# Kernel tuning notes

Hardware: AMD Instinct MI355X
Metric: run time of the kernel (lower is better)

The kernel has to match this reference:

```python
import jax, jax.numpy as jnp
import numpy as np
from jax import lax

B, H, W = 128, 128, 128
CHANS = [3, 32, 64, 128]   # convolution_structure
F, FH, FW = 128, 16, 16    # n_features, feature map size after 3 maxpools
P = FH * FW                # flatten_feature_size = 256
E, OUT = 32, 53            # expert_output_len, output_len


def _conv(x, w, b):
    # NCHW conv, 3x3, SAME padding, stride 1
    y = lax.conv_general_dilated(x, w, (1, 1), 'SAME',
                                 dimension_numbers=('NCHW', 'OIHW', 'NCHW'))
    return y + b[None, :, None, None]


def _maxpool2(x):
    return lax.reduce_window(x, -jnp.inf, lax.max,
                             (1, 1, 2, 2), (1, 1, 2, 2), 'VALID')


def setup_inputs() -> dict:
    key = jax.random.key(0)
    ks = jax.random.split(key, 16)

    def n(k, shape, fan_in):
        return jax.random.normal(k, shape, jnp.float32) / np.float32(np.sqrt(fan_in))

    inp = {'x': jax.random.normal(ks[0], (B, CHANS[0], H, W), jnp.float32)}
    for i in range(3):
        cin, cout = CHANS[i], CHANS[i + 1]
        inp[f'cw{i + 1}'] = n(ks[1 + i], (cout, cin, 3, 3), cin * 9)
        inp[f'cb{i + 1}'] = jnp.zeros((cout,), jnp.float32)
    inp['Wa'] = n(ks[4], (F, P), P)
    inp['ba'] = jnp.zeros((F,), jnp.float32)
    # per-expert MLP 256 -> 256 -> 128 -> 32 (128 experts, batched)
    inp['ew1'] = n(ks[5], (F, 256, 256), 256)
    inp['eb1'] = jnp.zeros((F, 256), jnp.float32)
    inp['ew2'] = n(ks[6], (F, 256, 128), 256)
    inp['eb2'] = jnp.zeros((F, 128), jnp.float32)
    inp['ew3'] = n(ks[7], (F, 128, E), 128)
    inp['eb3'] = jnp.zeros((F, E), jnp.float32)
    inp['fw'] = n(ks[8], (F * E, OUT), F * E)
    inp['fb'] = jnp.zeros((OUT,), jnp.float32)
    return inp


def reference(x, cw1, cb1, cw2, cb2, cw3, cb3, Wa, ba,
              ew1, eb1, ew2, eb2, ew3, eb3, fw, fb):
    # CNNBlock: (conv3x3 + ReLU + maxpool2) x 3  -> [B, F, 16, 16]
    h = x
    for w, b in ((cw1, cb1), (cw2, cb2), (cw3, cb3)):
        h = _maxpool2(jax.nn.relu(_conv(h, w, b)))
    feat = h.reshape(h.shape[0], F, P)                        # [B, F, 256]

    # AttentionBlock: per-feature scalar gate (attention_value = 1)
    att = jax.nn.sigmoid(jnp.einsum('bfp,fp->bf', feat, Wa) + ba)[:, :, None]

    # Experts: 128 independent gated MLPs, batched as grouped GEMMs
    z = feat * att                                            # input gating
    z = jax.nn.relu(jnp.einsum('bfp,fpq->bfq', z, ew1) + eb1)
    z = jax.nn.relu(jnp.einsum('bfp,fpq->bfq', z, ew2) + eb2)
    z = jnp.einsum('bfp,fpq->bfq', z, ew3) + eb3              # [B, F, 32]

    # outer ReLU over stacked expert outputs, flatten, final dense (att=1)
    z = jax.nn.relu(z).reshape(z.shape[0], -1)                # [B, 4096]
    return z @ fw + fb                                        # [B, 53]
```

## Files before the change

kernel.cpp:

```cpp
#include <hip/hip_runtime.h>
#include <hip/hip_bf16.h>
#include <math.h>

#define NF 128
#define NP 256

typedef __attribute__((ext_vector_type(8))) short bf16x8;
typedef __attribute__((ext_vector_type(4))) short bf16x4;
typedef __attribute__((ext_vector_type(4))) float f32x4;

#define GLOBAL_AS __attribute__((address_space(1)))
#define LDS_AS __attribute__((address_space(3)))

__global__ void __launch_bounds__(256) packs_k(
    const float* __restrict__ cw1, const float* __restrict__ cw2,
    const float* __restrict__ cw3, const float* __restrict__ fw,
    __hip_bfloat16* __restrict__ wp1, __hip_bfloat16* __restrict__ wp2,
    __hip_bfloat16* __restrict__ wp3, float* __restrict__ fwt)
{
    const int bid = blockIdx.x, tid = threadIdx.x;
    if (bid < 8) {
        int i = bid * 256 + tid;
        if (i >= 2048) return;
        int s = i >> 10, co = (i >> 5) & 31, k = i & 31;
        int o = s * 8 + (k >> 2), ch = k & 3;
        float v = 0.f;
        if (o < 9 && ch < 3) v = cw1[(size_t)(co * 3 + ch) * 9 + o];
        wp1[i] = __float2bfloat16(v);
    } else if (bid < 80) {
        int i = (bid - 8) * 256 + tid;
        if (i >= 9 * 64 * 32) return;
        int o = i / 2048, r = i - o * 2048;
        int co = r >> 5, ci = r & 31;
        wp2[i] = __float2bfloat16(cw2[(size_t)(co * 32 + ci) * 9 + o]);
    } else if (bid < 368) {
        int i = (bid - 80) * 256 + tid;
        if (i >= 9 * 128 * 64) return;
        int o = i / 8192, r = i - o * 8192;
        int co = r >> 6, ci = r & 63;
        wp3[i] = __float2bfloat16(cw3[(size_t)(co * 64 + ci) * 9 + o]);
    } else {
        int i = (bid - 368) * 256 + tid;
        if (i >= 53 * 4096) return;
        int o = i >> 12, k = i & 4095;
        fwt[i] = fw[(size_t)k * 53 + o];
    }
}

__global__ void __launch_bounds__(256) tpack_k(const float* __restrict__ in,
                                               __hip_bfloat16* __restrict__ out,
                                               int P, int Q, int qtiles)
{
    const int f  = blockIdx.y;
    const int pt = blockIdx.x / qtiles, qt = blockIdx.x - pt * qtiles;
    __shared__ float t[32][33];
    const float* src = in + (size_t)f * P * Q;
    __hip_bfloat16* dst = out + (size_t)f * P * Q;
    const int rr = threadIdx.x >> 5, c = threadIdx.x & 31;
    #pragma unroll
    for (int i = 0; i < 4; ++i)
        t[rr + i * 8][c] = src[(size_t)(pt * 32 + rr + i * 8) * Q + qt * 32 + c];
    __syncthreads();
    #pragma unroll
    for (int i = 0; i < 4; ++i)
        dst[(size_t)(qt * 32 + rr + i * 8) * P + pt * 32 + c] =
            __float2bfloat16(t[c][rr + i * 8]);
}

__global__ void __launch_bounds__(256, 2) conv1_mfma(
    const float* __restrict__ x,
    const __hip_bfloat16* __restrict__ wp1,
    const float* __restrict__ bias,
    __hip_bfloat16* __restrict__ out)
{
    __shared__ char lds[14 * 130 * 8];
    const int rb  = blockIdx.x * 8;
    const int b   = blockIdx.z;
    const int tid = threadIdx.x;

    #pragma unroll
    for (int t = 0; t < 8; ++t) {
        int u = tid + t * 256;
        if (u < 14 * 130) {
            int px = u % 130, row = u / 130;
            int gy = rb + row - 1, gx = px - 1;
            unsigned short hv[4] = {0, 0, 0, 0};
            if (gy >= 0 && gy < 128 && gx >= 0 && gx < 128) {
                size_t base = (((size_t)b * 3) * 128 + gy) * 128 + gx;
                __hip_bfloat16 h0 = __float2bfloat16(x[base]);
                __hip_bfloat16 h1 = __float2bfloat16(x[base + 16384]);
                __hip_bfloat16 h2 = __float2bfloat16(x[base + 32768]);
                __builtin_memcpy(&hv[0], &h0, 2);
                __builtin_memcpy(&hv[1], &h1, 2);
                __builtin_memcpy(&hv[2], &h2, 2);
            }
            *(int2*)(lds + u * 8) = *(const int2*)hv;
        }
    }
    __syncthreads();

    const int w = tid >> 6, lane = tid & 63, p = lane & 15, q = lane >> 4;

    f32x4 acc[16][2];
    #pragma unroll
    for (int m = 0; m < 16; ++m)
        #pragma unroll
        for (int n = 0; n < 2; ++n) {
            acc[m][n][0] = 0.f; acc[m][n][1] = 0.f;
            acc[m][n][2] = 0.f; acc[m][n][3] = 0.f;
        }

    #pragma unroll
    for (int s = 0; s < 2; ++s) {
        bf16x8 bfr[2];
        #pragma unroll
        for (int n = 0; n < 2; ++n)
            bfr[n] = *(const bf16x8*)(wp1 + (size_t)(s * 32 + n * 16 + p) * 32 + q * 8);
        const int o0 = s * 8 + q * 2, o1 = o0 + 1;
        const int dy0 = o0 / 3, dx0 = o0 - 3 * dy0;
        const int dy1 = o1 / 3, dx1 = o1 - 3 * dy1;
        #pragma unroll
        for (int m = 0; m < 16; ++m) {
            const int mr = m >> 3, mx = m & 7;
            const int r0 = (2 * w + mr + dy0) * 130 + mx * 16 + p + dx0;
            const int r1 = (2 * w + mr + dy1) * 130 + mx * 16 + p + dx1;
            bf16x4 lo = *(const bf16x4*)(lds + r0 * 8);
            bf16x4 hi = *(const bf16x4*)(lds + r1 * 8);
            bf16x8 afr = __builtin_shufflevector(lo, hi, 0, 1, 2, 3, 4, 5, 6, 7);
            #pragma unroll
            for (int n = 0; n < 2; ++n)
                acc[m][n] = __builtin_amdgcn_mfma_f32_16x16x32_bf16(afr, bfr[n], acc[m][n], 0, 0, 0);
        }
    }

    const int prow = (rb >> 1) + w;
    float bv[2] = { bias[p], bias[16 + p] };
    #pragma unroll
    for (int mx = 0; mx < 8; ++mx)
        #pragma unroll
        for (int n = 0; n < 2; ++n) {
            f32x4 lo = acc[mx][n], hi = acc[8 + mx][n];
            float v0 = fmaxf(fmaxf(fmaxf(lo[0], lo[1]), fmaxf(hi[0], hi[1])) + bv[n], 0.f);
            float v1 = fmaxf(fmaxf(fmaxf(lo[2], lo[3]), fmaxf(hi[2], hi[3])) + bv[n], 0.f);
            int px = mx * 8 + q * 2;
            size_t base = ((size_t)(b * 64 + prow) * 64 + px) * 32 + n * 16 + p;
            out[base]      = __float2bfloat16(v0);
            out[base + 32] = __float2bfloat16(v1);
        }
}

template<int W, int CIN, int COUT, int SWZ, int OUTF>
__global__ void __launch_bounds__(256, 2) conv_mfma(
    const __hip_bfloat16* __restrict__ in,
    const __hip_bfloat16* __restrict__ wp,
    const float* __restrict__ bias,
    __hip_bfloat16* __restrict__ outb,
    float* __restrict__ outf)
{
    constexpr int XW  = W / 16;
    constexpr int AF  = 2 * XW;
    constexpr int BF  = COUT / 16;
    constexpr int CH  = CIN / 8;
    constexpr int KH  = CIN / 32;
    constexpr int NSTEP = 9 * KH;
    constexpr int PXW = W + 2;
    constexpr int UNITS  = 10 * PXW * CH;
    constexpr int NIT    = (UNITS + 255) / 256;
    constexpr int STAGEB = UNITS * 16;
    constexpr int OUTLDS = OUTF ? (COUT * 68 * 4) : 0;
    constexpr int LDSB   = STAGEB > OUTLDS ? STAGEB : OUTLDS;

    __shared__ int4 ldsv[(LDSB + 15) / 16];
    char* ldsc = (char*)ldsv;

    const int rb  = blockIdx.x * 8;
    const int b   = blockIdx.z;
    const int tid = threadIdx.x;
    const int w = tid >> 6, lane = tid & 63, p = lane & 15, q = lane >> 4;

    #pragma unroll
    for (int t = 0; t < NIT; ++t) {
        int u = tid + t * 256;
        if (u < UNITS) {
            int ch = u % CH; int pl = u / CH;
            int xx = pl % PXW; int row = pl / PXW;
            int gy = rb + row - 1, gx = xx - 1;
            if (gy >= 0 && gy < W && gx >= 0 && gx < W) {
                int ch_src = SWZ ? (ch ^ (pl & 7)) : ch;
                const __hip_bfloat16* gp = in + ((size_t)(b * W + gy) * W + gx) * CIN + ch_src * 8;
                char* lb = ldsc + (size_t)(t * 256 + (tid & ~63)) * 16;
                __builtin_amdgcn_global_load_lds(
                    (const GLOBAL_AS void*)gp, (LDS_AS void*)lb, 16, 0, 0);
            } else {
                *(int4*)(ldsc + (size_t)u * 16) = make_int4(0, 0, 0, 0);
            }
        }
    }

    bf16x8 bcur[BF], bnxt[BF];
    #pragma unroll
    for (int n = 0; n < BF; ++n)
        bcur[n] = *(const bf16x8*)(wp + (size_t)(n * 16 + p) * CIN + q * 8);

    __syncthreads();

    f32x4 acc[AF][BF];
    #pragma unroll
    for (int m = 0; m < AF; ++m)
        #pragma unroll
        for (int n = 0; n < BF; ++n) {
            acc[m][n][0] = 0.f; acc[m][n][1] = 0.f;
            acc[m][n][2] = 0.f; acc[m][n][3] = 0.f;
        }

    float bv[BF];
    #pragma unroll
    for (int n = 0; n < BF; ++n) bv[n] = bias[n * 16 + p];

    #pragma unroll 1
    for (int s = 0; s < NSTEP; ++s) {
        const int o  = (KH == 1) ? s : (s >> 1);
        const int h  = (KH == 1) ? 0 : (s & 1);
        const int ky = o / 3, kx = o - 3 * (o / 3);

        if (s + 1 < NSTEP) {
            const int o2 = (KH == 1) ? (s + 1) : ((s + 1) >> 1);
            const int h2 = (KH == 1) ? 0 : ((s + 1) & 1);
            #pragma unroll
            for (int n = 0; n < BF; ++n)
                bnxt[n] = *(const bf16x8*)(wp + (size_t)(o2 * COUT + n * 16 + p) * CIN + h2 * 32 + q * 8);
        }

        bf16x8 afr[AF];
        #pragma unroll
        for (int m = 0; m < AF; ++m) {
            const int mr = m / XW, mx = m % XW;
            const int pix = (2 * w + mr + ky) * PXW + mx * 16 + kx + p;
            const int ch = h * 4 + q;
            const int slot = SWZ ? (pix * CH + (ch ^ (pix & 7))) : (pix * CH + ch);
            afr[m] = *(const bf16x8*)(ldsc + slot * 16);
        }
        #pragma unroll
        for (int m = 0; m < AF; ++m)
            #pragma unroll
            for (int n = 0; n < BF; ++n)
                acc[m][n] = __builtin_amdgcn_mfma_f32_16x16x32_bf16(afr[m], bcur[n], acc[m][n], 0, 0, 0);

        #pragma unroll
        for (int n = 0; n < BF; ++n) bcur[n] = bnxt[n];
    }

    const int prow = (rb >> 1) + w;
    if constexpr (OUTF == 0) {
        #pragma unroll
        for (int mx = 0; mx < XW; ++mx)
            #pragma unroll
            for (int n = 0; n < BF; ++n) {
                f32x4 lo = acc[mx][n], hi = acc[XW + mx][n];
                float v0 = fmaxf(fmaxf(fmaxf(lo[0], lo[1]), fmaxf(hi[0], hi[1])) + bv[n], 0.f);
                float v1 = fmaxf(fmaxf(fmaxf(lo[2], lo[3]), fmaxf(hi[2], hi[3])) + bv[n], 0.f);
                int px = mx * 8 + q * 2;
                size_t base = ((size_t)(b * (W / 2) + prow) * (W / 2) + px) * COUT + n * 16 + p;
                outb[base]        = __float2bfloat16(v0);
                outb[base + COUT] = __float2bfloat16(v1);
            }
    } else {
        __syncthreads();
        float* fl = (float*)ldsc;
        #pragma unroll
        for (int mx = 0; mx < XW; ++mx)
            #pragma unroll
            for (int n = 0; n < BF; ++n) {
                f32x4 lo = acc[mx][n], hi = acc[XW + mx][n];
                float v0 = fmaxf(fmaxf(fmaxf(lo[0], lo[1]), fmaxf(hi[0], hi[1])) + bv[n], 0.f);
                float v1 = fmaxf(fmaxf(fmaxf(lo[2], lo[3]), fmaxf(hi[2], hi[3])) + bv[n], 0.f);
                int px = mx * 8 + q * 2;
                fl[(n * 16 + p) * 68 + w * 16 + px]     = v0;
                fl[(n * 16 + p) * 68 + w * 16 + px + 1] = v1;
            }
        __syncthreads();
        for (int i = tid; i < COUT * 16; i += 256) {
            int c = i >> 4, j4 = i & 15;
            float4 vv = *(const float4*)&fl[c * 68 + j4 * 4];
            *(float4*)(outf + (size_t)(b * COUT + c) * 256 + (rb >> 1) * 16 + j4 * 4) = vv;
        }
    }
}

__global__ void __launch_bounds__(256, 2) experts_mfma(
    const float* __restrict__ feat, const float* __restrict__ Wa,
    const float* __restrict__ ba,
    const __hip_bfloat16* __restrict__ w1, const float* __restrict__ eb1,
    const __hip_bfloat16* __restrict__ w2, const float* __restrict__ eb2,
    const __hip_bfloat16* __restrict__ w3, const float* __restrict__ eb3,
    float* __restrict__ z)
{
    const int f  = blockIdx.x;
    const int r0 = blockIdx.y * 32;
    const int tid = threadIdx.x;

    __shared__ __attribute__((aligned(16))) char lds[33024];
    char* Xb  = lds;
    char* H1b = lds + 16384;
    char* H2b = lds;
    float* attL = (float*)(lds + 32768);

    for (int u = tid; u < 32 * 32; u += 256) {
        int row = u >> 5, ch = u & 31;
        int b = r0 + row;
        const float* src = feat + ((size_t)b * NF + f) * NP + ch * 8;
        float4 v0 = *(const float4*)src;
        float4 v1 = *(const float4*)(src + 4);
        unsigned short hv[8];
        float vv[8] = {v0.x, v0.y, v0.z, v0.w, v1.x, v1.y, v1.z, v1.w};
        #pragma unroll
        for (int j = 0; j < 8; ++j) {
            __hip_bfloat16 hb = __float2bfloat16(vv[j]);
            __builtin_memcpy(&hv[j], &hb, 2);
        }
        int slot = row * 32 + (ch ^ (row & 7));
        *(int4*)(Xb + slot * 16) = *(const int4*)hv;
    }

    {
        int row = tid >> 3, g = tid & 7;
        const float* fr = feat + ((size_t)(r0 + row) * NF + f) * NP + g * 32;
        const float* wr = Wa + (size_t)f * NP + g * 32;
        float s = 0.f;
        #pragma unroll
        for (int j = 0; j < 32; j += 4) {
            float4 a  = *(const float4*)(fr + j);
            float4 w4 = *(const float4*)(wr + j);
            s += a.x * w4.x + a.y * w4.y + a.z * w4.z + a.w * w4.w;
        }
        s += __shfl_xor(s, 1);
        s += __shfl_xor(s, 2);
        s += __shfl_xor(s, 4);
        if (g == 0) attL[row] = 1.f / (1.f + expf(-(s + ba[f])));
    }
    __syncthreads();

    const int wv = tid >> 6, lane = tid & 63, p = lane & 15, q = lane >> 4;
    const int rh = wv & 1, cf = wv >> 1;
    const int mrow = rh * 16;

    f32x4 acc1[8];
    #pragma unroll
    for (int n = 0; n < 8; ++n) { acc1[n][0]=0.f; acc1[n][1]=0.f; acc1[n][2]=0.f; acc1[n][3]=0.f; }
    #pragma unroll
    for (int k = 0; k < 8; ++k) {
        bf16x8 bfr[8];
        #pragma unroll
        for (int n = 0; n < 8; ++n)
            bfr[n] = *(const bf16x8*)(w1 + ((size_t)f * 256 + cf * 128 + n * 16 + p) * 256 + k * 32 + q * 8);
        int row = mrow + p, ch = k * 4 + q;
        bf16x8 afr = *(const bf16x8*)(Xb + (row * 32 + (ch ^ (row & 7))) * 16);
        #pragma unroll
        for (int n = 0; n < 8; ++n)
            acc1[n] = __builtin_amdgcn_mfma_f32_16x16x32_bf16(afr, bfr[n], acc1[n], 0, 0, 0);
    }
    #pragma unroll
    for (int n = 0; n < 8; ++n) {
        int col = cf * 128 + n * 16 + p;
        float bb = eb1[(size_t)f * 256 + col];
        #pragma unroll
        for (int reg = 0; reg < 4; ++reg) {
            int row = mrow + q * 4 + reg;
            float v = fmaxf(attL[row] * acc1[n][reg] + bb, 0.f);
            int slot = row * 32 + ((col >> 3) ^ (row & 7));
            *(__hip_bfloat16*)(H1b + slot * 16 + (col & 7) * 2) = __float2bfloat16(v);
        }
    }
    __syncthreads();

    f32x4 acc2[4];
    #pragma unroll
    for (int n = 0; n < 4; ++n) { acc2[n][0]=0.f; acc2[n][1]=0.f; acc2[n][2]=0.f; acc2[n][3]=0.f; }
    #pragma unroll
    for (int k = 0; k < 8; ++k) {
        bf16x8 bfr[4];
        #pragma unroll
        for (int n = 0; n < 4; ++n)
            bfr[n] = *(const bf16x8*)(w2 + ((size_t)f * 128 + cf * 64 + n * 16 + p) * 256 + k * 32 + q * 8);
        int row = mrow + p, ch = k * 4 + q;
        bf16x8 afr = *(const bf16x8*)(H1b + (row * 32 + (ch ^ (row & 7))) * 16);
        #pragma unroll
        for (int n = 0; n < 4; ++n)
            acc2[n] = __builtin_amdgcn_mfma_f32_16x16x32_bf16(afr, bfr[n], acc2[n], 0, 0, 0);
    }
    #pragma unroll
    for (int n = 0; n < 4; ++n) {
        int col = cf * 64 + n * 16 + p;
        float bb = eb2[(size_t)f * 128 + col];
        #pragma unroll
        for (int reg = 0; reg < 4; ++reg) {
            float v = fmaxf(acc2[n][reg] + bb, 0.f);
            int row = mrow + q * 4 + reg;
            int slot = row * 16 + ((col >> 3) ^ (row & 7));
            *(__hip_bfloat16*)(H2b + slot * 16 + (col & 7) * 2) = __float2bfloat16(v);
        }
    }
    __syncthreads();

    f32x4 acc3;
    acc3[0]=0.f; acc3[1]=0.f; acc3[2]=0.f; acc3[3]=0.f;
    #pragma unroll
    for (int k = 0; k < 4; ++k) {
        bf16x8 bfr = *(const bf16x8*)(w3 + ((size_t)f * 32 + cf * 16 + p) * 128 + k * 32 + q * 8);
        int row = mrow + p, ch = k * 4 + q;
        bf16x8 afr = *(const bf16x8*)(H2b + (row * 16 + (ch ^ (row & 7))) * 16);
        acc3 = __builtin_amdgcn_mfma_f32_16x16x32_bf16(afr, bfr, acc3, 0, 0, 0);
    }
    {
        float bb = eb3[(size_t)f * 32 + cf * 16 + p];
        #pragma unroll
        for (int reg = 0; reg < 4; ++reg) {
            float v = fmaxf(acc3[reg] + bb, 0.f);
            int row = r0 + mrow + q * 4 + reg;
            z[(size_t)row * 4096 + f * 32 + cf * 16 + p] = v;
        }
    }
}

__global__ void __launch_bounds__(256) final_k(
    const float* __restrict__ z, const float* __restrict__ fwt,
    const float* __restrict__ fb, float* __restrict__ out)
{
    const int b  = blockIdx.x;
    const int og = blockIdx.y;
    __shared__ float zs[4096];
    for (int i = threadIdx.x; i < 1024; i += 256)
        *(float4*)&zs[i * 4] = *(const float4*)&z[(size_t)b * 4096 + i * 4];
    __syncthreads();

    const int wv = threadIdx.x >> 6, lane = threadIdx.x & 63;
    const int o = og * 4 + wv;
    if (o >= 53) return;
    const float4* wr = (const float4*)&fwt[(size_t)o * 4096];
    float s = 0.f;
    #pragma unroll
    for (int it = 0; it < 16; ++it) {
        float4 zv = *(const float4*)&zs[(it * 64 + lane) * 4];
        float4 w4 = wr[it * 64 + lane];
        s += zv.x * w4.x + zv.y * w4.y + zv.z * w4.z + zv.w * w4.w;
    }
    #pragma unroll
    for (int off = 32; off; off >>= 1) s += __shfl_down(s, off);
    if (lane == 0) out[b * 53 + o] = s + fb[o];
}

extern "C" void kernel_launch(void* const* d_in, const int* in_sizes, int n_in,
                              void* d_out, int out_size, void* d_ws, size_t ws_size,
                              hipStream_t stream)
{
    const float* x   = (const float*)d_in[0];
    const float* cw1 = (const float*)d_in[1];
    const float* cb1 = (const float*)d_in[2];
    const float* cw2 = (const float*)d_in[3];
    const float* cb2 = (const float*)d_in[4];
    const float* cw3 = (const float*)d_in[5];
    const float* cb3 = (const float*)d_in[6];
    const float* Wa  = (const float*)d_in[7];
    const float* ba  = (const float*)d_in[8];
    const float* ew1 = (const float*)d_in[9];
    const float* eb1 = (const float*)d_in[10];
    const float* ew2 = (const float*)d_in[11];
    const float* eb2 = (const float*)d_in[12];
    const float* ew3 = (const float*)d_in[13];
    const float* eb3 = (const float*)d_in[14];
    const float* fw  = (const float*)d_in[15];
    const float* fb  = (const float*)d_in[16];

    float* ws = (float*)d_ws;
    __hip_bfloat16* p1b  = (__hip_bfloat16*)ws;
    __hip_bfloat16* p2b  = (__hip_bfloat16*)(ws + 8388608);
    float* feat = ws + 12582912;
    __hip_bfloat16* wp2  = (__hip_bfloat16*)(ws + 16793600);
    __hip_bfloat16* wp3  = (__hip_bfloat16*)(ws + 16802816);
    __hip_bfloat16* ew1b = (__hip_bfloat16*)(ws + 16839680);
    __hip_bfloat16* ew2b = (__hip_bfloat16*)(ws + 21033984);
    __hip_bfloat16* ew3b = (__hip_bfloat16*)(ws + 23131136);
    float* fwt = ws + 23393280;
    __hip_bfloat16* wp1b = (__hip_bfloat16*)(ws + 23610368);
    float* z   = ws;

    packs_k<<<1216, 256, 0, stream>>>(cw1, cw2, cw3, fw, wp1b, wp2, wp3, fwt);
    tpack_k<<<dim3(64, 128), 256, 0, stream>>>(ew1, ew1b, 256, 256, 8);
    tpack_k<<<dim3(32, 128), 256, 0, stream>>>(ew2, ew2b, 256, 128, 4);
    tpack_k<<<dim3(4, 128), 256, 0, stream>>>(ew3, ew3b, 128, 32, 1);

    conv1_mfma<<<dim3(16, 1, 128), 256, 0, stream>>>(x, wp1b, cb1, p1b);
    conv_mfma<64, 32, 64, 0, 0><<<dim3(8, 1, 128), 256, 0, stream>>>(p1b, wp2, cb2, p2b, nullptr);
    conv_mfma<32, 64, 128, 1, 1><<<dim3(4, 1, 128), 256, 0, stream>>>(p2b, wp3, cb3, nullptr, feat);
    experts_mfma<<<dim3(128, 4), 256, 0, stream>>>(feat, Wa, ba, ew1b, eb1, ew2b, eb2, ew3b, eb3, z);
    final_k<<<dim3(128, 14), 256, 0, stream>>>(z, fwt, fb, (float*)d_out);
}
```

Measured before the change: 152.3 us.

## Merge weight-packing launches and widen expert tiles to 64 rows per block

```diff
diff --git a/kernel.cpp b/kernel.cpp
--- a/kernel.cpp
+++ b/kernel.cpp
@@ -12,12 +12,33 @@
 #define GLOBAL_AS __attribute__((address_space(1)))
 #define LDS_AS __attribute__((address_space(3)))
 
+__device__ __forceinline__ void tpack_tile(const float* __restrict__ src,
+                                           __hip_bfloat16* __restrict__ dst,
+                                           int P, int Q, int pt, int qt,
+                                           int tid, float (*t)[33])
+{
+    const int rr = tid >> 5, c = tid & 31;
+    #pragma unroll
+    for (int i = 0; i < 4; ++i)
+        t[rr + i * 8][c] = src[(size_t)(pt * 32 + rr + i * 8) * Q + qt * 32 + c];
+    __syncthreads();
+    #pragma unroll
+    for (int i = 0; i < 4; ++i)
+        dst[(size_t)(qt * 32 + rr + i * 8) * P + pt * 32 + c] =
+            __float2bfloat16(t[c][rr + i * 8]);
+}
+
 __global__ void __launch_bounds__(256) packs_k(
     const float* __restrict__ cw1, const float* __restrict__ cw2,
     const float* __restrict__ cw3, const float* __restrict__ fw,
+    const float* __restrict__ ew1, const float* __restrict__ ew2,
+    const float* __restrict__ ew3,
     __hip_bfloat16* __restrict__ wp1, __hip_bfloat16* __restrict__ wp2,
-    __hip_bfloat16* __restrict__ wp3, float* __restrict__ fwt)
-{
+    __hip_bfloat16* __restrict__ wp3, float* __restrict__ fwt,
+    __hip_bfloat16* __restrict__ ew1b, __hip_bfloat16* __restrict__ ew2b,
+    __hip_bfloat16* __restrict__ ew3b)
+{
+    __shared__ float t[32][33];
     const int bid = blockIdx.x, tid = threadIdx.x;
     if (bid < 8) {
         int i = bid * 256 + tid;
@@ -39,32 +60,27 @@
         int o = i / 8192, r = i - o * 8192;
         int co = r >> 6, ci = r & 63;
         wp3[i] = __float2bfloat16(cw3[(size_t)(co * 64 + ci) * 9 + o]);
-    } else {
+    } else if (bid < 1216) {
         int i = (bid - 368) * 256 + tid;
         if (i >= 53 * 4096) return;
         int o = i >> 12, k = i & 4095;
         fwt[i] = fw[(size_t)k * 53 + o];
-    }
-}
-
-__global__ void __launch_bounds__(256) tpack_k(const float* __restrict__ in,
-                                               __hip_bfloat16* __restrict__ out,
-                                               int P, int Q, int qtiles)
-{
-    const int f  = blockIdx.y;
-    const int pt = blockIdx.x / qtiles, qt = blockIdx.x - pt * qtiles;
-    __shared__ float t[32][33];
-    const float* src = in + (size_t)f * P * Q;
-    __hip_bfloat16* dst = out + (size_t)f * P * Q;
-    const int rr = threadIdx.x >> 5, c = threadIdx.x & 31;
-    #pragma unroll
-    for (int i = 0; i < 4; ++i)
-        t[rr + i * 8][c] = src[(size_t)(pt * 32 + rr + i * 8) * Q + qt * 32 + c];
-    __syncthreads();
-    #pragma unroll
-    for (int i = 0; i < 4; ++i)
-        dst[(size_t)(qt * 32 + rr + i * 8) * P + pt * 32 + c] =
-            __float2bfloat16(t[c][rr + i * 8]);
+    } else if (bid < 9408) {
+        int r = bid - 1216;
+        int f = r >> 6, tile = r & 63;
+        tpack_tile(ew1 + (size_t)f * 65536, ew1b + (size_t)f * 65536,
+                   256, 256, tile >> 3, tile & 7, tid, t);
+    } else if (bid < 13504) {
+        int r = bid - 9408;
+        int f = r >> 5, tile = r & 31;
+        tpack_tile(ew2 + (size_t)f * 32768, ew2b + (size_t)f * 32768,
+                   256, 128, tile >> 2, tile & 3, tid, t);
+    } else {
+        int r = bid - 13504;
+        int f = r >> 2, tile = r & 3;
+        tpack_tile(ew3 + (size_t)f * 4096, ew3b + (size_t)f * 4096,
+                   128, 32, tile, 0, tid, t);
+    }
 }
 
 __global__ void __launch_bounds__(256, 2) conv1_mfma(
@@ -296,16 +312,17 @@
     float* __restrict__ z)
 {
     const int f  = blockIdx.x;
-    const int r0 = blockIdx.y * 32;
+    const int r0 = blockIdx.y * 64;
     const int tid = threadIdx.x;
 
-    __shared__ __attribute__((aligned(16))) char lds[33024];
+    __shared__ __attribute__((aligned(16))) char lds[65536];
     char* Xb  = lds;
-    char* H1b = lds + 16384;
+    char* H1b = lds + 32768;
     char* H2b = lds;
-    float* attL = (float*)(lds + 32768);
-
-    for (int u = tid; u < 32 * 32; u += 256) {
+
+    #pragma unroll
+    for (int t = 0; t < 8; ++t) {
+        int u = tid + t * 256;
         int row = u >> 5, ch = u & 31;
         int b = r0 + row;
         const float* src = feat + ((size_t)b * NF + f) * NP + ch * 8;
@@ -322,75 +339,76 @@
         *(int4*)(Xb + slot * 16) = *(const int4*)hv;
     }
 
+    const int wv = tid >> 6, lane = tid & 63, p = lane & 15, q = lane >> 4;
+    const int mrow = wv * 16;
+
+    float att_val;
     {
-        int row = tid >> 3, g = tid & 7;
-        const float* fr = feat + ((size_t)(r0 + row) * NF + f) * NP + g * 32;
-        const float* wr = Wa + (size_t)f * NP + g * 32;
+        int rl = lane >> 2, sub = lane & 3;
+        const float* fr = feat + ((size_t)(r0 + mrow + rl) * NF + f) * NP + sub * 64;
+        const float* wr = Wa + (size_t)f * NP + sub * 64;
         float s = 0.f;
         #pragma unroll
-        for (int j = 0; j < 32; j += 4) {
+        for (int j = 0; j < 64; j += 4) {
             float4 a  = *(const float4*)(fr + j);
             float4 w4 = *(const float4*)(wr + j);
             s += a.x * w4.x + a.y * w4.y + a.z * w4.z + a.w * w4.w;
         }
         s += __shfl_xor(s, 1);
         s += __shfl_xor(s, 2);
-        s += __shfl_xor(s, 4);
-        if (g == 0) attL[row] = 1.f / (1.f + expf(-(s + ba[f])));
-    }
-    __syncthreads();
-
-    const int wv = tid >> 6, lane = tid & 63, p = lane & 15, q = lane >> 4;
-    const int rh = wv & 1, cf = wv >> 1;
-    const int mrow = rh * 16;
-
-    f32x4 acc1[8];
-    #pragma unroll
-    for (int n = 0; n < 8; ++n) { acc1[n][0]=0.f; acc1[n][1]=0.f; acc1[n][2]=0.f; acc1[n][3]=0.f; }
+        att_val = 1.f / (1.f + expf(-(s + ba[f])));
+    }
+    __syncthreads();
+
+    f32x4 acc1[16];
+    #pragma unroll
+    for (int n = 0; n < 16; ++n) { acc1[n][0]=0.f; acc1[n][1]=0.f; acc1[n][2]=0.f; acc1[n][3]=0.f; }
+    #pragma unroll
+    for (int k = 0; k < 8; ++k) {
+        bf16x8 bfr[16];
+        #pragma unroll
+        for (int n = 0; n < 16; ++n)
+            bfr[n] = *(const bf16x8*)(w1 + ((size_t)f * 256 + n * 16 + p) * 256 + k * 32 + q * 8);
+        int row = mrow + p, ch = k * 4 + q;
+        bf16x8 afr = *(const bf16x8*)(Xb + (row * 32 + (ch ^ (row & 7))) * 16);
+        #pragma unroll
+        for (int n = 0; n < 16; ++n)
+            acc1[n] = __builtin_amdgcn_mfma_f32_16x16x32_bf16(afr, bfr[n], acc1[n], 0, 0, 0);
+    }
+    #pragma unroll
+    for (int n = 0; n < 16; ++n) {
+        int col = n * 16 + p;
+        float bb = eb1[(size_t)f * 256 + col];
+        #pragma unroll
+        for (int reg = 0; reg < 4; ++reg) {
+            int rowl = q * 4 + reg;
+            float av = __shfl(att_val, wv * 64 >= 0 ? (rowl << 2) : 0);
+            float v = fmaxf(av * acc1[n][reg] + bb, 0.f);
+            int row = mrow + rowl;
+            int slot = row * 32 + ((col >> 3) ^ (row & 7));
+            *(__hip_bfloat16*)(H1b + slot * 16 + (col & 7) * 2) = __float2bfloat16(v);
+        }
+    }
+    __syncthreads();
+
+    f32x4 acc2[8];
+    #pragma unroll
+    for (int n = 0; n < 8; ++n) { acc2[n][0]=0.f; acc2[n][1]=0.f; acc2[n][2]=0.f; acc2[n][3]=0.f; }
     #pragma unroll
     for (int k = 0; k < 8; ++k) {
         bf16x8 bfr[8];
         #pragma unroll
         for (int n = 0; n < 8; ++n)
-            bfr[n] = *(const bf16x8*)(w1 + ((size_t)f * 256 + cf * 128 + n * 16 + p) * 256 + k * 32 + q * 8);
-        int row = mrow + p, ch = k * 4 + q;
-        bf16x8 afr = *(const bf16x8*)(Xb + (row * 32 + (ch ^ (row & 7))) * 16);
-        #pragma unroll
-        for (int n = 0; n < 8; ++n)
-            acc1[n] = __builtin_amdgcn_mfma_f32_16x16x32_bf16(afr, bfr[n], acc1[n], 0, 0, 0);
-    }
-    #pragma unroll
-    for (int n = 0; n < 8; ++n) {
-        int col = cf * 128 + n * 16 + p;
-        float bb = eb1[(size_t)f * 256 + col];
-        #pragma unroll
-        for (int reg = 0; reg < 4; ++reg) {
-            int row = mrow + q * 4 + reg;
-            float v = fmaxf(attL[row] * acc1[n][reg] + bb, 0.f);
-            int slot = row * 32 + ((col >> 3) ^ (row & 7));
-            *(__hip_bfloat16*)(H1b + slot * 16 + (col & 7) * 2) = __float2bfloat16(v);
-        }
-    }
-    __syncthreads();
-
-    f32x4 acc2[4];
-    #pragma unroll
-    for (int n = 0; n < 4; ++n) { acc2[n][0]=0.f; acc2[n][1]=0.f; acc2[n][2]=0.f; acc2[n][3]=0.f; }
-    #pragma unroll
-    for (int k = 0; k < 8; ++k) {
-        bf16x8 bfr[4];
-        #pragma unroll
-        for (int n = 0; n < 4; ++n)
-            bfr[n] = *(const bf16x8*)(w2 + ((size_t)f * 128 + cf * 64 + n * 16 + p) * 256 + k * 32 + q * 8);
+            bfr[n] = *(const bf16x8*)(w2 + ((size_t)f * 128 + n * 16 + p) * 256 + k * 32 + q * 8);
         int row = mrow + p, ch = k * 4 + q;
         bf16x8 afr = *(const bf16x8*)(H1b + (row * 32 + (ch ^ (row & 7))) * 16);
         #pragma unroll
-        for (int n = 0; n < 4; ++n)
+        for (int n = 0; n < 8; ++n)
             acc2[n] = __builtin_amdgcn_mfma_f32_16x16x32_bf16(afr, bfr[n], acc2[n], 0, 0, 0);
     }
     #pragma unroll
-    for (int n = 0; n < 4; ++n) {
-        int col = cf * 64 + n * 16 + p;
+    for (int n = 0; n < 8; ++n) {
+        int col = n * 16 + p;
         float bb = eb2[(size_t)f * 128 + col];
         #pragma unroll
         for (int reg = 0; reg < 4; ++reg) {
@@ -402,22 +420,29 @@
     }
     __syncthreads();
 
-    f32x4 acc3;
-    acc3[0]=0.f; acc3[1]=0.f; acc3[2]=0.f; acc3[3]=0.f;
+    f32x4 acc3[2];
+    #pragma unroll
+    for (int n = 0; n < 2; ++n) { acc3[n][0]=0.f; acc3[n][1]=0.f; acc3[n][2]=0.f; acc3[n][3]=0.f; }
     #pragma unroll
     for (int k = 0; k < 4; ++k) {
-        bf16x8 bfr = *(const bf16x8*)(w3 + ((size_t)f * 32 + cf * 16 + p) * 128 + k * 32 + q * 8);
+        bf16x8 bfr[2];
+        #pragma unroll
+        for (int n = 0; n < 2; ++n)
+            bfr[n] = *(const bf16x8*)(w3 + ((size_t)f * 32 + n * 16 + p) * 128 + k * 32 + q * 8);
         int row = mrow + p, ch = k * 4 + q;
         bf16x8 afr = *(const bf16x8*)(H2b + (row * 16 + (ch ^ (row & 7))) * 16);
-        acc3 = __builtin_amdgcn_mfma_f32_16x16x32_bf16(afr, bfr, acc3, 0, 0, 0);
-    }
-    {
-        float bb = eb3[(size_t)f * 32 + cf * 16 + p];
+        #pragma unroll
+        for (int n = 0; n < 2; ++n)
+            acc3[n] = __builtin_amdgcn_mfma_f32_16x16x32_bf16(afr, bfr[n], acc3[n], 0, 0, 0);
+    }
+    #pragma unroll
+    for (int n = 0; n < 2; ++n) {
+        float bb = eb3[(size_t)f * 32 + n * 16 + p];
         #pragma unroll
         for (int reg = 0; reg < 4; ++reg) {
-            float v = fmaxf(acc3[reg] + bb, 0.f);
+            float v = fmaxf(acc3[n][reg] + bb, 0.f);
             int row = r0 + mrow + q * 4 + reg;
-            z[(size_t)row * 4096 + f * 32 + cf * 16 + p] = v;
+            z[(size_t)row * 4096 + f * 32 + n * 16 + p] = v;
         }
     }
 }
@@ -484,14 +509,12 @@
     __hip_bfloat16* wp1b = (__hip_bfloat16*)(ws + 23610368);
     float* z   = ws;
 
-    packs_k<<<1216, 256, 0, stream>>>(cw1, cw2, cw3, fw, wp1b, wp2, wp3, fwt);
-    tpack_k<<<dim3(64, 128), 256, 0, stream>>>(ew1, ew1b, 256, 256, 8);
-    tpack_k<<<dim3(32, 128), 256, 0, stream>>>(ew2, ew2b, 256, 128, 4);
-    tpack_k<<<dim3(4, 128), 256, 0, stream>>>(ew3, ew3b, 128, 32, 1);
+    packs_k<<<14016, 256, 0, stream>>>(cw1, cw2, cw3, fw, ew1, ew2, ew3,
+                                       wp1b, wp2, wp3, fwt, ew1b, ew2b, ew3b);
 
     conv1_mfma<<<dim3(16, 1, 128), 256, 0, stream>>>(x, wp1b, cb1, p1b);
     conv_mfma<64, 32, 64, 0, 0><<<dim3(8, 1, 128), 256, 0, stream>>>(p1b, wp2, cb2, p2b, nullptr);
     conv_mfma<32, 64, 128, 1, 1><<<dim3(4, 1, 128), 256, 0, stream>>>(p2b, wp3, cb3, nullptr, feat);
-    experts_mfma<<<dim3(128, 4), 256, 0, stream>>>(feat, Wa, ba, ew1b, eb1, ew2b, eb2, ew3b, eb3, z);
+    experts_mfma<<<dim3(128, 2), 256, 0, stream>>>(feat, Wa, ba, ew1b, eb1, ew2b, eb2, ew3b, eb3, z);
     final_k<<<dim3(128, 14), 256, 0, stream>>>(z, fwt, fb, (float*)d_out);
 }
```

Result: no change. 149.4 us (-1.9%).
